# Optimization experiments

Measured on AMD Instinct MI355X. Metric: run time of the kernel, lower is better.

Reference implementation:

```python
import jax, jax.numpy as jnp
import numpy as np
from jax import lax

DIM = 512
D_STATE = 16
D_CONV = 4
EXPAND = 2
E = EXPAND * DIM  # expanded_dim


def setup_inputs() -> dict:
    key = jax.random.key(0)
    ks = jax.random.split(key, 8)
    B_, L = 4, 2048
    x = jax.random.normal(ks[0], (B_, L, DIM), dtype=jnp.float32)
    # parameters (xavier-ish scaled random; exact init values don't matter for math)
    W_in = jax.random.normal(ks[1], (2 * E, DIM), dtype=jnp.float32) * (1.0 / np.sqrt(DIM))
    W_conv = jax.random.normal(ks[2], (E, 1, D_CONV), dtype=jnp.float32) * 0.3
    A = jax.random.normal(ks[3], (E, D_STATE), dtype=jnp.float32) * 0.5
    Bp = jax.random.normal(ks[4], (E, D_STATE), dtype=jnp.float32) * (1.0 / np.sqrt(D_STATE))
    Cp = jax.random.normal(ks[5], (E, D_STATE), dtype=jnp.float32) * (1.0 / np.sqrt(D_STATE))
    Dp = jnp.zeros((E,), dtype=jnp.float32)
    W_out = jax.random.normal(ks[6], (DIM, E), dtype=jnp.float32) * (1.0 / np.sqrt(E))
    return {"x": x, "W_in": W_in, "W_conv": W_conv, "A": A, "Bp": Bp, "Cp": Cp, "Dp": Dp, "W_out": W_out}


def reference(x, W_in, W_conv, A, Bp, Cp, Dp, W_out):
    residual = x
    b, l, _ = x.shape
    xp = jnp.einsum('bld,ed->ble', x, W_in)        # [b,l,2E]
    xs, gate = jnp.split(xp, 2, axis=-1)
    xs = xs * jax.nn.sigmoid(gate)                 # [b,l,E]
    # causal depthwise conv1d: torch pads both sides by K-1 then slices [:, :, :l]
    xc = lax.conv_general_dilated(
        xs.transpose(0, 2, 1), W_conv,
        window_strides=(1,), padding=[(D_CONV - 1, 0)],
        feature_group_count=E,
        dimension_numbers=('NCH', 'OIH', 'NCH'))     # [b,E,l]
    u = jax.nn.silu(xc.transpose(0, 2, 1))          # [b,l,E]
    Aneg = -jnp.exp(A)                              # [E,N]
    delta = jax.nn.sigmoid(jnp.einsum('bld,dn->bln', u, Bp))  # [b,l,N]
    A_bar = jnp.exp(jnp.einsum('dn,bln->bldn', Aneg, delta))  # [b,l,E,N]
    Bx = jnp.einsum('bln,dn->bldn', delta, Bp) * u[..., None]  # B_bar * x_t

    def step(h, inp):
        A_t, Bx_t = inp
        h = A_t * h + Bx_t                          # [b,E,N]
        y_t = jnp.einsum('bdn,dn->bd', h, Cp)
        return h, y_t

    h0 = jnp.zeros((b, E, D_STATE), dtype=x.dtype)
    _, ys = lax.scan(step, h0, (A_bar.transpose(1, 0, 2, 3), Bx.transpose(1, 0, 2, 3)))
    y = ys.transpose(1, 0, 2)                       # [b,l,E]
    y = y + Dp * u
    out = jnp.einsum('ble,de->bld', y, W_out)
    return out + residual
```

## Files before the change

kernel.cpp:

```cpp
#include <hip/hip_runtime.h>

#define DIM   512
#define EE    1024
#define NS    16
#define BB    4
#define LL    2048
#define MM    (BB*LL)
#define NC    32
#define CL    64

typedef __bf16 bf16x8 __attribute__((ext_vector_type(8)));
typedef __bf16 bf16x4 __attribute__((ext_vector_type(4)));
typedef float  f32x4  __attribute__((ext_vector_type(4)));
typedef _Float16 f16x8 __attribute__((ext_vector_type(8)));

static __device__ __forceinline__ float sigmoidf_(float x) {
    return 1.0f / (1.0f + __expf(-x));
}

#define GLOAD(gp, lp) __builtin_amdgcn_global_load_lds( \
    (const __attribute__((address_space(1))) unsigned int*)(const void*)(gp), \
    (__attribute__((address_space(3))) unsigned int*)(void*)(lp), 16, 0, 0)

__global__ __launch_bounds__(256) void k_tobf(
    const float* __restrict__ x, const float* __restrict__ Win,
    const float* __restrict__ Wout, const float* __restrict__ Bp,
    __bf16* __restrict__ xbf, __bf16* __restrict__ winbf,
    __bf16* __restrict__ woutbf, __bf16* __restrict__ bpT)
{
    int g = blockIdx.x * 256 + threadIdx.x;
    const int nx4 = MM * DIM / 4;
    const int nw4 = 2 * EE * DIM / 4;
    const int no4 = DIM * EE / 4;
    if (g < nx4) {
        f32x4 v = ((const f32x4*)x)[g];
        bf16x4 o; for (int j = 0; j < 4; ++j) o[j] = (__bf16)v[j];
        ((bf16x4*)xbf)[g] = o;
    } else if (g < nx4 + nw4) {
        int i = g - nx4;
        f32x4 v = ((const f32x4*)Win)[i];
        bf16x4 o; for (int j = 0; j < 4; ++j) o[j] = (__bf16)v[j];
        ((bf16x4*)winbf)[i] = o;
    } else if (g < nx4 + nw4 + no4) {
        int i = g - nx4 - nw4;
        f32x4 v = ((const f32x4*)Wout)[i];
        bf16x4 o; for (int j = 0; j < 4; ++j) o[j] = (__bf16)v[j];
        ((bf16x4*)woutbf)[i] = o;
    } else {
        int i = g - nx4 - nw4 - no4;
        int e = i >> 4, n = i & 15;
        bpT[n * EE + e] = (__bf16)Bp[i];
    }
}

__global__ __launch_bounds__(256, 4) void k_gemm1(
    const __bf16* __restrict__ Abf,
    const __bf16* __restrict__ Wbf,
    __bf16* __restrict__ xs)
{
    __shared__ __bf16 sA[128 * 64];
    __shared__ __bf16 sB0[64 * 64];
    __shared__ __bf16 sB1[64 * 64];

    int bid = blockIdx.x;
    int swz = (bid & 7) * 128 + (bid >> 3);
    int bm = swz >> 4;
    int bn = swz & 15;

    int t = threadIdx.x;
    int lane = t & 63;
    int w = t >> 6;
    int wm = (w >> 1) * 64;
    int wn = (w & 1) * 32;
    int r15 = lane & 15;
    int kq = lane >> 4;

    const __bf16* Agb  = Abf + (bm * 128) * DIM;
    const __bf16* B0gb = Wbf + (bn * 64) * DIM;
    const __bf16* B1gb = Wbf + (1024 + bn * 64) * DIM;

    f32x4 accx[4][2] = {};
    f32x4 accg[4][2] = {};

    for (int kt = 0; kt < 8; ++kt) {
        #pragma unroll
        for (int i_ = 0; i_ < 4; ++i_) {
            int c_ = i_ * 256 + t;
            int row_ = c_ >> 3;
            int ss_ = (c_ & 7) ^ (row_ & 7);
            GLOAD(Agb + kt * 64 + row_ * DIM + ss_ * 8, sA + (i_ * 256 + w * 64) * 8);
        }
        #pragma unroll
        for (int i_ = 0; i_ < 2; ++i_) {
            int c_ = i_ * 256 + t;
            int row_ = c_ >> 3;
            int ss_ = (c_ & 7) ^ (row_ & 7);
            GLOAD(B0gb + kt * 64 + row_ * DIM + ss_ * 8, sB0 + (i_ * 256 + w * 64) * 8);
            GLOAD(B1gb + kt * 64 + row_ * DIM + ss_ * 8, sB1 + (i_ * 256 + w * 64) * 8);
        }
        __syncthreads();
        #pragma unroll
        for (int ks = 0; ks < 2; ++ks) {
            int kcs = ks * 4 + kq;
            bf16x8 a[4], b0[2], b1[2];
            #pragma unroll
            for (int m = 0; m < 4; ++m) {
                int r = wm + m * 16 + r15;
                a[m] = *(const bf16x8*)&sA[r * 64 + (kcs ^ (r & 7)) * 8];
            }
            #pragma unroll
            for (int n = 0; n < 2; ++n) {
                int r = wn + n * 16 + r15;
                b0[n] = *(const bf16x8*)&sB0[r * 64 + (kcs ^ (r & 7)) * 8];
                b1[n] = *(const bf16x8*)&sB1[r * 64 + (kcs ^ (r & 7)) * 8];
            }
            #pragma unroll
            for (int m = 0; m < 4; ++m)
                #pragma unroll
                for (int n = 0; n < 2; ++n) {
                    accx[m][n] = __builtin_amdgcn_mfma_f32_16x16x32_bf16(a[m], b0[n], accx[m][n], 0, 0, 0);
                    accg[m][n] = __builtin_amdgcn_mfma_f32_16x16x32_bf16(a[m], b1[n], accg[m][n], 0, 0, 0);
                }
        }
        __syncthreads();
    }

    #pragma unroll
    for (int m = 0; m < 4; ++m)
        #pragma unroll
        for (int n = 0; n < 2; ++n)
            #pragma unroll
            for (int r = 0; r < 4; ++r) {
                int row = bm * 128 + wm + m * 16 + (lane >> 4) * 4 + r;
                int col = bn * 64 + wn + n * 16 + r15;
                float xv = accx[m][n][r];
                float gv = accg[m][n][r];
                xs[row * EE + col] = (__bf16)(xv * sigmoidf_(gv));
            }
}

__global__ __launch_bounds__(256) void k_convdelta(
    const __bf16* __restrict__ xs, const float* __restrict__ Wc,
    const __bf16* __restrict__ bpT,
    __bf16* __restrict__ u, float* __restrict__ delta)
{
    __shared__ __bf16 uS[8][1032];
    __shared__ float red[4][256];
    int bid = blockIdx.x;
    int r0b = bid * 8;
    int t = threadIdx.x;
    int cg_ = t & 127, rh = t >> 7;
    int e8 = cg_ << 3;
    int rr0 = r0b + rh * 4;
    int l0 = rr0 & (LL - 1);

    f32x4 wj[8];
    #pragma unroll
    for (int j = 0; j < 8; ++j) wj[j] = *(const f32x4*)&Wc[(e8 + j) * 4];
    bf16x8 z = {};
    bf16x8 win[7];
    #pragma unroll
    for (int i = 0; i < 7; ++i) {
        win[i] = (l0 + i >= 3) ? *(const bf16x8*)&xs[(rr0 + i - 3) * EE + e8] : z;
    }
    #pragma unroll
    for (int i = 0; i < 4; ++i) {
        bf16x8 out;
        #pragma unroll
        for (int j = 0; j < 8; ++j) {
            float a = (float)win[i][j] * wj[j][0] + (float)win[i + 1][j] * wj[j][1]
                    + (float)win[i + 2][j] * wj[j][2] + (float)win[i + 3][j] * wj[j][3];
            out[j] = (__bf16)(a * sigmoidf_(a));
        }
        *(bf16x8*)&u[(rr0 + i) * EE + e8] = out;
        *(bf16x8*)&uS[rh * 4 + i][e8] = out;
    }
    __syncthreads();

    int lane = t & 63, w = t >> 6;
    int ar = lane & 15, kc = (lane >> 4) << 3;
    f32x4 acc = {};
    #pragma unroll
    for (int k0 = 0; k0 < 256; k0 += 32) {
        int k = w * 256 + k0 + kc;
        bf16x8 a = *(const bf16x8*)&uS[ar & 7][k];
        bf16x8 b = *(const bf16x8*)&bpT[ar * EE + k];
        acc = __builtin_amdgcn_mfma_f32_16x16x32_bf16(a, b, acc, 0, 0, 0);
    }
    *(f32x4*)&red[w][lane * 4] = acc;
    __syncthreads();
    if (t < 32) {
        #pragma unroll
        for (int r = 0; r < 4; ++r) {
            float s = red[0][t * 4 + r] + red[1][t * 4 + r]
                    + red[2][t * 4 + r] + red[3][t * 4 + r];
            int row = (t >> 4) * 4 + r;
            int col = t & 15;
            delta[(r0b + row) * NS + col] = sigmoidf_(s);
        }
    }
}

__global__ __launch_bounds__(256) void k_scan1(
    const __bf16* __restrict__ u, const float* __restrict__ delta,
    const float* __restrict__ A, const float* __restrict__ Bp,
    const float* __restrict__ Cp, const float* __restrict__ Dp,
    _Float16* __restrict__ hbuf, float* __restrict__ Dsum,
    __bf16* __restrict__ yloc)
{
    int bid = blockIdx.x;
    int et = bid & 3;
    int c  = (bid >> 2) & (NC - 1);
    int b  = bid >> 7;
    int t  = threadIdx.x;
    int e  = et * 256 + t;
    __shared__ float dls[CL * NS];
    int sbase = (b * LL + c * CL) * NS;
    for (int i = t; i < CL * NS; i += 256) dls[i] = delta[sbase + i];
    __syncthreads();

    if (et == 0 && t < NS) {
        float s = 0.f;
        #pragma unroll
        for (int l = 0; l < CL; ++l) s += dls[l * NS + t];
        Dsum[(b * NC + c) * NS + t] = s;
    }

    float Ae[NS], Bpr[NS], Cr[NS];
    #pragma unroll
    for (int q = 0; q < 4; ++q) {
        f32x4 av = *(const f32x4*)&A[e * NS + q * 4];
        f32x4 bv = *(const f32x4*)&Bp[e * NS + q * 4];
        f32x4 cv = *(const f32x4*)&Cp[e * NS + q * 4];
        #pragma unroll
        for (int j = 0; j < 4; ++j) {
            Ae[q * 4 + j]  = -__expf(av[j]) * 1.44269504f;
            Bpr[q * 4 + j] = bv[j];
            Cr[q * 4 + j]  = cv[j];
        }
    }
    float Dv = Dp[e];
    float h[NS] = {};
    const __bf16* up = &u[(b * LL + c * CL) * EE + e];
    __bf16* yp = &yloc[(b * LL + c * CL) * EE + e];
    for (int l = 0; l < CL; ++l) {
        float uv = (float)up[l * EE];
        float yv = Dv * uv;
        const f32x4* dr = (const f32x4*)&dls[l * NS];
        f32x4 dv[4] = {dr[0], dr[1], dr[2], dr[3]};
        #pragma unroll
        for (int j = 0; j < NS; ++j) {
            float d  = dv[j >> 2][j & 3];
            float ab = __builtin_amdgcn_exp2f(Ae[j] * d);
            h[j] = ab * h[j] + (d * Bpr[j]) * uv;
            yv += h[j] * Cr[j];
        }
        yp[l * EE] = (__bf16)yv;
    }
    int base = ((b * NC + c) * EE + e) * NS;
    f16x8 h0, h1;
    #pragma unroll
    for (int j = 0; j < 8; ++j) { h0[j] = (_Float16)h[j]; h1[j] = (_Float16)h[8 + j]; }
    *(f16x8*)&hbuf[base] = h0;
    *(f16x8*)&hbuf[base + 8] = h1;
}

__global__ __launch_bounds__(256) void k_fix(
    const float* __restrict__ A, const float* __restrict__ Dsum,
    _Float16* __restrict__ hbuf)
{
    int g = blockIdx.x * 256 + threadIdx.x;
    int b = g >> 14;
    int r = g & 16383;
    int n = r & 15;
    float Ae = -__expf(A[r]) * 1.44269504f;
    float h = 0.f;
    for (int c = 0; c < NC; ++c) {
        int idx = (b * NC + c) * (EE * NS) + r;
        float hl = (float)hbuf[idx];
        float P  = __builtin_amdgcn_exp2f(Ae * Dsum[(b * NC + c) * NS + n]);
        hbuf[idx] = (_Float16)h;
        h = P * h + hl;
    }
}

__global__ __launch_bounds__(256) void k_scan2(
    const float* __restrict__ delta, const float* __restrict__ A,
    const float* __restrict__ Cp, const _Float16* __restrict__ hin,
    __bf16* __restrict__ y)
{
    int bid = blockIdx.x;
    int et = bid & 3;
    int c  = (bid >> 2) & (NC - 1);
    int b  = bid >> 7;
    if (c == 0) return;
    int t  = threadIdx.x;
    int e  = et * 256 + t;
    __shared__ float dls[CL * NS];
    int sbase = (b * LL + c * CL) * NS;
    for (int i = t; i < CL * NS; i += 256) dls[i] = delta[sbase + i];
    __syncthreads();

    int base = ((b * NC + c) * EE + e) * NS;
    f16x8 hv0 = *(const f16x8*)&hin[base];
    f16x8 hv1 = *(const f16x8*)&hin[base + 8];
    float Ae[NS], g_[NS];
    #pragma unroll
    for (int q = 0; q < 4; ++q) {
        f32x4 av = *(const f32x4*)&A[e * NS + q * 4];
        f32x4 cv = *(const f32x4*)&Cp[e * NS + q * 4];
        #pragma unroll
        for (int j = 0; j < 4; ++j) {
            int jj = q * 4 + j;
            Ae[jj] = -__expf(av[j]) * 1.44269504f;
            float hvv = (jj < 8) ? (float)hv0[jj & 7] : (float)hv1[jj & 7];
            g_[jj] = cv[j] * hvv;
        }
    }
    float D[NS] = {};
    __bf16* yp = &y[(b * LL + c * CL) * EE + e];
    for (int l = 0; l < CL; ++l) {
        const f32x4* dr = (const f32x4*)&dls[l * NS];
        f32x4 dv[4] = {dr[0], dr[1], dr[2], dr[3]};
        float corr = 0.f;
        #pragma unroll
        for (int j = 0; j < NS; ++j) {
            D[j] += dv[j >> 2][j & 3];
            corr += g_[j] * __builtin_amdgcn_exp2f(Ae[j] * D[j]);
        }
        float yv = (float)yp[l * EE] + corr;
        yp[l * EE] = (__bf16)yv;
    }
}

__global__ __launch_bounds__(256, 2) void k_gemm2(
    const __bf16* __restrict__ Ybf,
    const __bf16* __restrict__ Wobf,
    const __bf16* __restrict__ xres,
    float* __restrict__ out)
{
    __shared__ __bf16 sA[128 * 64];
    __shared__ __bf16 sB[64 * 64];

    int bid = blockIdx.x;
    int swz = (bid & 7) * 64 + (bid >> 3);
    int bm = swz >> 3;
    int bn = swz & 7;

    int t = threadIdx.x;
    int lane = t & 63;
    int w = t >> 6;
    int wm = (w >> 1) * 64;
    int wn = (w & 1) * 32;
    int r15 = lane & 15;
    int kq = lane >> 4;

    const __bf16* Agb = Ybf + (bm * 128) * EE;
    const __bf16* Bgb = Wobf + (bn * 64) * EE;

    f32x4 acc[4][2] = {};

    for (int kt = 0; kt < 16; ++kt) {
        #pragma unroll
        for (int i_ = 0; i_ < 4; ++i_) {
            int c_ = i_ * 256 + t;
            int row_ = c_ >> 3;
            int ss_ = (c_ & 7) ^ (row_ & 7);
            GLOAD(Agb + kt * 64 + row_ * EE + ss_ * 8, sA + (i_ * 256 + w * 64) * 8);
        }
        #pragma unroll
        for (int i_ = 0; i_ < 2; ++i_) {
            int c_ = i_ * 256 + t;
            int row_ = c_ >> 3;
            int ss_ = (c_ & 7) ^ (row_ & 7);
            GLOAD(Bgb + kt * 64 + row_ * EE + ss_ * 8, sB + (i_ * 256 + w * 64) * 8);
        }
        __syncthreads();
        #pragma unroll
        for (int ks = 0; ks < 2; ++ks) {
            int kcs = ks * 4 + kq;
            bf16x8 a[4], bfr[2];
            #pragma unroll
            for (int m = 0; m < 4; ++m) {
                int r = wm + m * 16 + r15;
                a[m] = *(const bf16x8*)&sA[r * 64 + (kcs ^ (r & 7)) * 8];
            }
            #pragma unroll
            for (int n = 0; n < 2; ++n) {
                int r = wn + n * 16 + r15;
                bfr[n] = *(const bf16x8*)&sB[r * 64 + (kcs ^ (r & 7)) * 8];
            }
            #pragma unroll
            for (int m = 0; m < 4; ++m)
                #pragma unroll
                for (int n = 0; n < 2; ++n)
                    acc[m][n] = __builtin_amdgcn_mfma_f32_16x16x32_bf16(a[m], bfr[n], acc[m][n], 0, 0, 0);
        }
        __syncthreads();
    }

    #pragma unroll
    for (int m = 0; m < 4; ++m)
        #pragma unroll
        for (int n = 0; n < 2; ++n)
            #pragma unroll
            for (int r = 0; r < 4; ++r) {
                int row = bm * 128 + wm + m * 16 + (lane >> 4) * 4 + r;
                int col = bn * 64 + wn + n * 16 + r15;
                out[row * DIM + col] = acc[m][n][r] + (float)xres[row * DIM + col];
            }
}

extern "C" void kernel_launch(void* const* d_in, const int* in_sizes, int n_in,
                              void* d_out, int out_size, void* d_ws, size_t ws_size,
                              hipStream_t stream) {
    const float* x    = (const float*)d_in[0];
    const float* Win  = (const float*)d_in[1];
    const float* Wc   = (const float*)d_in[2];
    const float* A    = (const float*)d_in[3];
    const float* Bp   = (const float*)d_in[4];
    const float* Cp   = (const float*)d_in[5];
    const float* Dp   = (const float*)d_in[6];
    const float* Wout = (const float*)d_in[7];

    char* ws = (char*)d_ws;
    __bf16* woutbf = (__bf16*)(ws + 0);
    __bf16* bpT    = (__bf16*)(ws + 1048576);
    float*  delta  = (float*)(ws + 1081344);
    float*  Dsum   = (float*)(ws + 1605632);
    __bf16* ubf    = (__bf16*)(ws + 1622016);
    __bf16* xbf    = (__bf16*)(ws + 18399232);
    __bf16* winbf  = (__bf16*)(ws + 26787840);
    __bf16* xsbf   = (__bf16*)(ws + 28884992);
    __bf16* yloc   = (__bf16*)(ws + 28884992);
    _Float16* hbuf = (_Float16*)(ws + 45662208);

    k_tobf     <<<5696, 256, 0, stream>>>(x, Win, Wout, Bp, xbf, winbf, woutbf, bpT);
    k_gemm1    <<<1024, 256, 0, stream>>>(xbf, winbf, xsbf);
    k_convdelta<<<1024, 256, 0, stream>>>(xsbf, Wc, bpT, ubf, delta);
    k_scan1    <<<512, 256, 0, stream>>>(ubf, delta, A, Bp, Cp, Dp, hbuf, Dsum, yloc);
    k_fix      <<<256, 256, 0, stream>>>(A, Dsum, hbuf);
    k_scan2    <<<512, 256, 0, stream>>>(delta, A, Cp, hbuf, yloc);
    k_gemm2    <<<512, 256, 0, stream>>>(yloc, woutbf, xbf, (float*)d_out);
}
```

Measured before the change: 149.9 us.

## Split scan state dimension across 4 lanes and halve chunk length

The chunked scan kernels now give each channel's 16 state entries to 4 threads (4 states each) and combine the per-timestep outputs with warp shuffles. Chunk length drops from 64 to 32 with 64 chunks, so grids grow from 512 to 4096 blocks. The aim is more parallelism and a shorter serial dependency chain per thread on a low-occupancy scan. In exchange it adds shuffle reductions, redundant u loads per lane, strided single-lane bf16 stores, and twice as many chunks to walk in the sequential k_fix pass. The hbuf and Dsum buffer sizes double with NC, and it is not visible whether the workspace offsets allow for that.

```diff
diff --git a/kernel.cpp b/kernel.cpp
--- a/kernel.cpp
+++ b/kernel.cpp
@@ -6,13 +6,13 @@
 #define BB    4
 #define LL    2048
 #define MM    (BB*LL)
-#define NC    32
-#define CL    64
+#define NC    64
+#define CL    32
 
 typedef __bf16 bf16x8 __attribute__((ext_vector_type(8)));
 typedef __bf16 bf16x4 __attribute__((ext_vector_type(4)));
 typedef float  f32x4  __attribute__((ext_vector_type(4)));
-typedef _Float16 f16x8 __attribute__((ext_vector_type(8)));
+typedef _Float16 f16x4 __attribute__((ext_vector_type(4)));
 
 static __device__ __forceinline__ float sigmoidf_(float x) {
     return 1.0f / (1.0f + __expf(-x));
@@ -209,60 +209,61 @@
     __bf16* __restrict__ yloc)
 {
     int bid = blockIdx.x;
-    int et = bid & 3;
-    int c  = (bid >> 2) & (NC - 1);
-    int b  = bid >> 7;
+    int eblk = bid & 15;
+    int c  = (bid >> 4) & (NC - 1);
+    int b  = bid >> 10;
     int t  = threadIdx.x;
-    int e  = et * 256 + t;
+    int elocal = t >> 2;
+    int ng = t & 3;
+    int e  = eblk * 64 + elocal;
     __shared__ float dls[CL * NS];
     int sbase = (b * LL + c * CL) * NS;
     for (int i = t; i < CL * NS; i += 256) dls[i] = delta[sbase + i];
     __syncthreads();
 
-    if (et == 0 && t < NS) {
+    if (eblk == 0 && t < NS) {
         float s = 0.f;
         #pragma unroll
         for (int l = 0; l < CL; ++l) s += dls[l * NS + t];
         Dsum[(b * NC + c) * NS + t] = s;
     }
 
-    float Ae[NS], Bpr[NS], Cr[NS];
-    #pragma unroll
-    for (int q = 0; q < 4; ++q) {
-        f32x4 av = *(const f32x4*)&A[e * NS + q * 4];
-        f32x4 bv = *(const f32x4*)&Bp[e * NS + q * 4];
-        f32x4 cv = *(const f32x4*)&Cp[e * NS + q * 4];
+    float Ae[4], Bpr[4], Cr[4];
+    {
+        f32x4 av = *(const f32x4*)&A[e * NS + ng * 4];
+        f32x4 bv = *(const f32x4*)&Bp[e * NS + ng * 4];
+        f32x4 cv = *(const f32x4*)&Cp[e * NS + ng * 4];
         #pragma unroll
         for (int j = 0; j < 4; ++j) {
-            Ae[q * 4 + j]  = -__expf(av[j]) * 1.44269504f;
-            Bpr[q * 4 + j] = bv[j];
-            Cr[q * 4 + j]  = cv[j];
+            Ae[j]  = -__expf(av[j]) * 1.44269504f;
+            Bpr[j] = bv[j];
+            Cr[j]  = cv[j];
         }
     }
     float Dv = Dp[e];
-    float h[NS] = {};
+    float h[4] = {};
     const __bf16* up = &u[(b * LL + c * CL) * EE + e];
     __bf16* yp = &yloc[(b * LL + c * CL) * EE + e];
     for (int l = 0; l < CL; ++l) {
         float uv = (float)up[l * EE];
-        float yv = Dv * uv;
-        const f32x4* dr = (const f32x4*)&dls[l * NS];
-        f32x4 dv[4] = {dr[0], dr[1], dr[2], dr[3]};
-        #pragma unroll
-        for (int j = 0; j < NS; ++j) {
-            float d  = dv[j >> 2][j & 3];
+        f32x4 dv = *(const f32x4*)&dls[l * NS + ng * 4];
+        float yv = 0.f;
+        #pragma unroll
+        for (int j = 0; j < 4; ++j) {
+            float d  = dv[j];
             float ab = __builtin_amdgcn_exp2f(Ae[j] * d);
             h[j] = ab * h[j] + (d * Bpr[j]) * uv;
             yv += h[j] * Cr[j];
         }
-        yp[l * EE] = (__bf16)yv;
-    }
-    int base = ((b * NC + c) * EE + e) * NS;
-    f16x8 h0, h1;
-    #pragma unroll
-    for (int j = 0; j < 8; ++j) { h0[j] = (_Float16)h[j]; h1[j] = (_Float16)h[8 + j]; }
-    *(f16x8*)&hbuf[base] = h0;
-    *(f16x8*)&hbuf[base + 8] = h1;
+        yv += __shfl_xor(yv, 1);
+        yv += __shfl_xor(yv, 2);
+        if (ng == 0) yp[l * EE] = (__bf16)(yv + Dv * uv);
+    }
+    int basep = ((b * NC + c) * EE + e) * NS + ng * 4;
+    f16x4 hv;
+    #pragma unroll
+    for (int j = 0; j < 4; ++j) hv[j] = (_Float16)h[j];
+    *(f16x4*)&hbuf[basep] = hv;
 }
 
 __global__ __launch_bounds__(256) void k_fix(
@@ -290,46 +291,47 @@
     __bf16* __restrict__ y)
 {
     int bid = blockIdx.x;
-    int et = bid & 3;
-    int c  = (bid >> 2) & (NC - 1);
-    int b  = bid >> 7;
+    int eblk = bid & 15;
+    int c  = (bid >> 4) & (NC - 1);
+    int b  = bid >> 10;
     if (c == 0) return;
     int t  = threadIdx.x;
-    int e  = et * 256 + t;
+    int elocal = t >> 2;
+    int ng = t & 3;
+    int e  = eblk * 64 + elocal;
     __shared__ float dls[CL * NS];
     int sbase = (b * LL + c * CL) * NS;
     for (int i = t; i < CL * NS; i += 256) dls[i] = delta[sbase + i];
     __syncthreads();
 
-    int base = ((b * NC + c) * EE + e) * NS;
-    f16x8 hv0 = *(const f16x8*)&hin[base];
-    f16x8 hv1 = *(const f16x8*)&hin[base + 8];
-    float Ae[NS], g_[NS];
-    #pragma unroll
-    for (int q = 0; q < 4; ++q) {
-        f32x4 av = *(const f32x4*)&A[e * NS + q * 4];
-        f32x4 cv = *(const f32x4*)&Cp[e * NS + q * 4];
+    int basep = ((b * NC + c) * EE + e) * NS + ng * 4;
+    f16x4 hv = *(const f16x4*)&hin[basep];
+    float Ae[4], g_[4];
+    {
+        f32x4 av = *(const f32x4*)&A[e * NS + ng * 4];
+        f32x4 cv = *(const f32x4*)&Cp[e * NS + ng * 4];
         #pragma unroll
         for (int j = 0; j < 4; ++j) {
-            int jj = q * 4 + j;
-            Ae[jj] = -__expf(av[j]) * 1.44269504f;
-            float hvv = (jj < 8) ? (float)hv0[jj & 7] : (float)hv1[jj & 7];
-            g_[jj] = cv[j] * hvv;
-        }
-    }
-    float D[NS] = {};
+            Ae[j] = -__expf(av[j]) * 1.44269504f;
+            g_[j] = cv[j] * (float)hv[j];
+        }
+    }
+    float D[4] = {};
     __bf16* yp = &y[(b * LL + c * CL) * EE + e];
     for (int l = 0; l < CL; ++l) {
-        const f32x4* dr = (const f32x4*)&dls[l * NS];
-        f32x4 dv[4] = {dr[0], dr[1], dr[2], dr[3]};
+        f32x4 dv = *(const f32x4*)&dls[l * NS + ng * 4];
         float corr = 0.f;
         #pragma unroll
-        for (int j = 0; j < NS; ++j) {
-            D[j] += dv[j >> 2][j & 3];
+        for (int j = 0; j < 4; ++j) {
+            D[j] += dv[j];
             corr += g_[j] * __builtin_amdgcn_exp2f(Ae[j] * D[j]);
         }
-        float yv = (float)yp[l * EE] + corr;
-        yp[l * EE] = (__bf16)yv;
+        corr += __shfl_xor(corr, 1);
+        corr += __shfl_xor(corr, 2);
+        if (ng == 0) {
+            float yv = (float)yp[l * EE] + corr;
+            yp[l * EE] = (__bf16)yv;
+        }
     }
 }
 
@@ -438,8 +440,8 @@
     k_tobf     <<<5696, 256, 0, stream>>>(x, Win, Wout, Bp, xbf, winbf, woutbf, bpT);
     k_gemm1    <<<1024, 256, 0, stream>>>(xbf, winbf, xsbf);
     k_convdelta<<<1024, 256, 0, stream>>>(xsbf, Wc, bpT, ubf, delta);
-    k_scan1    <<<512, 256, 0, stream>>>(ubf, delta, A, Bp, Cp, Dp, hbuf, Dsum, yloc);
+    k_scan1    <<<4096, 256, 0, stream>>>(ubf, delta, A, Bp, Cp, Dp, hbuf, Dsum, yloc);
     k_fix      <<<256, 256, 0, stream>>>(A, Dsum, hbuf);
-    k_scan2    <<<512, 256, 0, stream>>>(delta, A, Cp, hbuf, yloc);
+    k_scan2    <<<4096, 256, 0, stream>>>(delta, A, Cp, hbuf, yloc);
     k_gemm2    <<<512, 256, 0, stream>>>(yloc, woutbf, xbf, (float*)d_out);
 }
```

Measured after the change: 153.5 us. +2.4%, slower.

## Halve scan chunk length and stage scan u/y tiles through LDS

Applied to the files above, without the earlier changes.

Changes the chunked scan from 32 chunks of 64 tokens to 64 chunks of 32 tokens, doubling the blocks in both scan passes to raise occupancy. The scan kernels also load their u/y and delta tiles into LDS with global_load_lds and write results back as 16-byte vector stores, replacing strided 2-byte global accesses. In exchange, the carry buffer doubles in size and the serial k_fix pass over chunks gets twice as long. The added LDS use could also limit occupancy.

```diff
diff --git a/kernel.cpp b/kernel.cpp
--- a/kernel.cpp
+++ b/kernel.cpp
@@ -6,8 +6,8 @@
 #define BB    4
 #define LL    2048
 #define MM    (BB*LL)
-#define NC    32
-#define CL    64
+#define NC    64
+#define CL    32
 
 typedef __bf16 bf16x8 __attribute__((ext_vector_type(8)));
 typedef __bf16 bf16x4 __attribute__((ext_vector_type(4)));
@@ -201,29 +201,33 @@
     }
 }
 
-__global__ __launch_bounds__(256) void k_scan1(
+__global__ __launch_bounds__(256, 4) void k_scan1(
     const __bf16* __restrict__ u, const float* __restrict__ delta,
     const float* __restrict__ A, const float* __restrict__ Bp,
     const float* __restrict__ Cp, const float* __restrict__ Dp,
     _Float16* __restrict__ hbuf, float* __restrict__ Dsum,
     __bf16* __restrict__ yloc)
 {
+    __shared__ __bf16 uS[CL * 256];
+    __shared__ __bf16 yS[CL * 256];
+    __shared__ float dls[CL * NS];
     int bid = blockIdx.x;
     int et = bid & 3;
     int c  = (bid >> 2) & (NC - 1);
-    int b  = bid >> 7;
+    int b  = bid >> 8;
     int t  = threadIdx.x;
-    int e  = et * 256 + t;
-    __shared__ float dls[CL * NS];
-    int sbase = (b * LL + c * CL) * NS;
-    for (int i = t; i < CL * NS; i += 256) dls[i] = delta[sbase + i];
-    __syncthreads();
-
-    if (et == 0 && t < NS) {
-        float s = 0.f;
-        #pragma unroll
-        for (int l = 0; l < CL; ++l) s += dls[l * NS + t];
-        Dsum[(b * NC + c) * NS + t] = s;
+    int lane = t & 63, w = t >> 6;
+    int e0 = et * 256;
+    int tok0 = b * LL + c * CL;
+    int e  = e0 + t;
+
+    if (w < 2)
+        GLOAD(delta + tok0 * NS + w * 256 + lane * 4, dls + w * 256);
+    #pragma unroll
+    for (int i = 0; i < 4; ++i) {
+        int chunk = i * 256 + t;
+        GLOAD(u + (tok0 + (chunk >> 5)) * EE + e0 + (chunk & 31) * 8,
+              uS + (i * 256 + w * 64) * 8);
     }
 
     float Ae[NS], Bpr[NS], Cr[NS];
@@ -240,11 +244,18 @@
         }
     }
     float Dv = Dp[e];
+    __syncthreads();
+
+    if (et == 0 && t < NS) {
+        float s = 0.f;
+        #pragma unroll
+        for (int l = 0; l < CL; ++l) s += dls[l * NS + t];
+        Dsum[(b * NC + c) * NS + t] = s;
+    }
+
     float h[NS] = {};
-    const __bf16* up = &u[(b * LL + c * CL) * EE + e];
-    __bf16* yp = &yloc[(b * LL + c * CL) * EE + e];
     for (int l = 0; l < CL; ++l) {
-        float uv = (float)up[l * EE];
+        float uv = (float)uS[l * 256 + t];
         float yv = Dv * uv;
         const f32x4* dr = (const f32x4*)&dls[l * NS];
         f32x4 dv[4] = {dr[0], dr[1], dr[2], dr[3]};
@@ -255,14 +266,22 @@
             h[j] = ab * h[j] + (d * Bpr[j]) * uv;
             yv += h[j] * Cr[j];
         }
-        yp[l * EE] = (__bf16)yv;
-    }
-    int base = ((b * NC + c) * EE + e) * NS;
+        yS[l * 256 + t] = (__bf16)yv;
+    }
+    int basep = ((b * NC + c) * EE + e) * NS;
     f16x8 h0, h1;
     #pragma unroll
     for (int j = 0; j < 8; ++j) { h0[j] = (_Float16)h[j]; h1[j] = (_Float16)h[8 + j]; }
-    *(f16x8*)&hbuf[base] = h0;
-    *(f16x8*)&hbuf[base + 8] = h1;
+    *(f16x8*)&hbuf[basep] = h0;
+    *(f16x8*)&hbuf[basep + 8] = h1;
+
+    __syncthreads();
+    #pragma unroll
+    for (int i = 0; i < 4; ++i) {
+        int chunk = i * 256 + t;
+        *(bf16x8*)&yloc[(tok0 + (chunk >> 5)) * EE + e0 + (chunk & 31) * 8]
+            = *(const bf16x8*)&yS[chunk * 8];
+    }
 }
 
 __global__ __launch_bounds__(256) void k_fix(
@@ -284,7 +303,7 @@
     }
 }
 
-__global__ __launch_bounds__(256) void k_scan2(
+__global__ __launch_bounds__(256, 4) void k_scan2(
     const float* __restrict__ delta, const float* __restrict__ A,
     const float* __restrict__ Cp, const _Float16* __restrict__ hin,
     __bf16* __restrict__ y)
@@ -292,18 +311,28 @@
     int bid = blockIdx.x;
     int et = bid & 3;
     int c  = (bid >> 2) & (NC - 1);
-    int b  = bid >> 7;
+    int b  = bid >> 8;
     if (c == 0) return;
+    __shared__ __bf16 yS[CL * 256];
+    __shared__ float dls[CL * NS];
     int t  = threadIdx.x;
-    int e  = et * 256 + t;
-    __shared__ float dls[CL * NS];
-    int sbase = (b * LL + c * CL) * NS;
-    for (int i = t; i < CL * NS; i += 256) dls[i] = delta[sbase + i];
-    __syncthreads();
-
-    int base = ((b * NC + c) * EE + e) * NS;
-    f16x8 hv0 = *(const f16x8*)&hin[base];
-    f16x8 hv1 = *(const f16x8*)&hin[base + 8];
+    int lane = t & 63, w = t >> 6;
+    int e0 = et * 256;
+    int tok0 = b * LL + c * CL;
+    int e  = e0 + t;
+
+    if (w < 2)
+        GLOAD(delta + tok0 * NS + w * 256 + lane * 4, dls + w * 256);
+    #pragma unroll
+    for (int i = 0; i < 4; ++i) {
+        int chunk = i * 256 + t;
+        GLOAD(y + (tok0 + (chunk >> 5)) * EE + e0 + (chunk & 31) * 8,
+              yS + (i * 256 + w * 64) * 8);
+    }
+
+    int basep = ((b * NC + c) * EE + e) * NS;
+    f16x8 hv0 = *(const f16x8*)&hin[basep];
+    f16x8 hv1 = *(const f16x8*)&hin[basep + 8];
     float Ae[NS], g_[NS];
     #pragma unroll
     for (int q = 0; q < 4; ++q) {
@@ -317,8 +346,9 @@
             g_[jj] = cv[j] * hvv;
         }
     }
+    __syncthreads();
+
     float D[NS] = {};
-    __bf16* yp = &y[(b * LL + c * CL) * EE + e];
     for (int l = 0; l < CL; ++l) {
         const f32x4* dr = (const f32x4*)&dls[l * NS];
         f32x4 dv[4] = {dr[0], dr[1], dr[2], dr[3]};
@@ -328,8 +358,16 @@
             D[j] += dv[j >> 2][j & 3];
             corr += g_[j] * __builtin_amdgcn_exp2f(Ae[j] * D[j]);
         }
-        float yv = (float)yp[l * EE] + corr;
-        yp[l * EE] = (__bf16)yv;
+        int idx = l * 256 + t;
+        yS[idx] = (__bf16)((float)yS[idx] + corr);
+    }
+
+    __syncthreads();
+    #pragma unroll
+    for (int i = 0; i < 4; ++i) {
+        int chunk = i * 256 + t;
+        *(bf16x8*)&y[(tok0 + (chunk >> 5)) * EE + e0 + (chunk & 31) * 8]
+            = *(const bf16x8*)&yS[chunk * 8];
     }
 }
 
@@ -438,8 +476,8 @@
     k_tobf     <<<5696, 256, 0, stream>>>(x, Win, Wout, Bp, xbf, winbf, woutbf, bpT);
     k_gemm1    <<<1024, 256, 0, stream>>>(xbf, winbf, xsbf);
     k_convdelta<<<1024, 256, 0, stream>>>(xsbf, Wc, bpT, ubf, delta);
-    k_scan1    <<<512, 256, 0, stream>>>(ubf, delta, A, Bp, Cp, Dp, hbuf, Dsum, yloc);
+    k_scan1    <<<1024, 256, 0, stream>>>(ubf, delta, A, Bp, Cp, Dp, hbuf, Dsum, yloc);
     k_fix      <<<256, 256, 0, stream>>>(A, Dsum, hbuf);
-    k_scan2    <<<512, 256, 0, stream>>>(delta, A, Cp, hbuf, yloc);
+    k_scan2    <<<1024, 256, 0, stream>>>(delta, A, Cp, hbuf, yloc);
     k_gemm2    <<<512, 256, 0, stream>>>(yloc, woutbf, xbf, (float*)d_out);
 }
```

Result: faster. 139.4 us (-7.0%).
